# Performance work log

Measured on AMD Instinct MI355X. Metric: run time of the kernel, lower is better.

## Reference

```python
import jax, jax.numpy as jnp
import numpy as np
import math

D_MODEL = 256
SIGMA = 1.0


def _sinusoidal_pe(L, d_model, dtype=jnp.float32):
    # pe[l, 2i] = sin(l * w_i), pe[l, 2i+1] = cos(l * w_i)
    position = jnp.arange(L, dtype=dtype)[:, None]                       # [L,1]
    div_term = jnp.exp(jnp.arange(0, d_model, 2, dtype=dtype) * (-math.log(10000.0) / d_model))
    pe = jnp.zeros((L, d_model), dtype=dtype)
    pe = pe.at[:, 0::2].set(jnp.sin(position * div_term))
    pe = pe.at[:, 1::2].set(jnp.cos(position * div_term))
    return pe  # [L, d_model]


def setup_inputs() -> dict:
    key = jax.random.key(0)
    # scale 0.05 keeps pairwise sq-distances O(1) so S = exp(-d/2) is non-degenerate
    x = jax.random.normal(key, (4, 4096, 256), dtype=jnp.float32) * 0.05
    return {"x": x}


def reference(x):
    B, L, D = x.shape
    pe = _sinusoidal_pe(L, D_MODEL, dtype=x.dtype)[None]                 # [1,L,D]
    # pairwise squared distances via the expansion ||a||^2+||b||^2-2ab (avoids [B,L,L,D])
    sq = jnp.sum(x * x, axis=-1)                                         # [B,L]
    gram = jnp.einsum('bld,bmd->blm', x, x)                              # [B,L,L]
    dist_sq = jnp.maximum(sq[:, :, None] + sq[:, None, :] - 2.0 * gram, 0.0)
    S = jnp.exp(-dist_sq / (2.0 * SIGMA ** 2))                           # [B,L,L]
    sem = jnp.einsum('blm,bmd->bld', S, x) / jnp.sum(S, axis=-1, keepdims=True)
    return x + pe + sem
```

## Files before the change

kernel.cpp:

```cpp
#include <hip/hip_runtime.h>

typedef unsigned char u8;
typedef float f32x4 __attribute__((ext_vector_type(4)));
typedef float f32x16 __attribute__((ext_vector_type(16)));

#define LL 4096
#define PSTR 136
#define SCALE 16.0f
#define GSCALE (1.0f/256.0f)
#define FREQC (-0.03597789207803197f)

__device__ __forceinline__ long LCAST(uint2 v) { return __builtin_bit_cast(long, v); }

typedef __attribute__((address_space(3))) u8 lds_u8;
typedef __attribute__((address_space(1))) u8 glb_u8;
__device__ __forceinline__ void dma16(const u8* g, u8* l) {
  __builtin_amdgcn_global_load_lds((const glb_u8*)g, (lds_u8*)l, 16, 0, 0);
}

__global__ __launch_bounds__(256) void prep1(const float* __restrict__ x, u8* __restrict__ xbf,
                                             u8* __restrict__ xT, float* __restrict__ sq) {
  __shared__ u8 T[16 * 264];
  const int blk = blockIdx.x;
  const int b = blk >> 8, r0 = (blk & 255) << 4;
  const int tid = threadIdx.x;
  const long rowbase = (long)(b << 12) + r0;
  const float4* x4 = (const float4*)x + rowbase * 64;
  unsigned* xb4 = (unsigned*)xbf + rowbase * 64;
  #pragma unroll
  for (int i = 0; i < 4; ++i) {
    int idx = i * 256 + tid;
    float4 v = x4[idx];
    float s = v.x * v.x + v.y * v.y + v.z * v.z + v.w * v.w;
    #pragma unroll
    for (int o = 32; o; o >>= 1) s += __shfl_xor(s, o);
    int row = idx >> 6, dw = idx & 63;
    if ((tid & 63) == 0) sq[rowbase + row] = s;
    int pk = __builtin_amdgcn_cvt_pk_fp8_f32(v.x * SCALE, v.y * SCALE, 0, false);
    pk = __builtin_amdgcn_cvt_pk_fp8_f32(v.z * SCALE, v.w * SCALE, pk, true);
    int sdw = (((dw >> 1) ^ ((r0 + row) & 31)) << 1) | (dw & 1);
    xb4[row * 64 + sdw] = (unsigned)pk;
    *(unsigned*)(T + row * 264 + dw * 4) = (unsigned)pk;
  }
  __syncthreads();
  unsigned ob[4];
  #pragma unroll
  for (int jj = 0; jj < 4; ++jj) {
    unsigned b0 = T[(4 * jj + 0) * 264 + tid];
    unsigned b1 = T[(4 * jj + 1) * 264 + tid];
    unsigned b2 = T[(4 * jj + 2) * 264 + tid];
    unsigned b3 = T[(4 * jj + 3) * 264 + tid];
    ob[jj] = b0 | (b1 << 8) | (b2 << 16) | (b3 << 24);
  }
  u8* drow = xT + ((((long)(b << 8) + tid) << 12)) + ((r0 >> 7) << 7);
  const int cb = (r0 & 127) >> 3, key = tid & 15;
  *(uint2*)(drow + ((cb ^ key) << 3)) = *(uint2*)(ob);
  *(uint2*)(drow + (((cb + 1) ^ key) << 3)) = *(uint2*)(ob + 2);
}

__global__ __launch_bounds__(512, 2) void tpe_main(
    const u8* __restrict__ xbf, const u8* __restrict__ xT,
    const float* __restrict__ sqv,
    const float* __restrict__ x, float* __restrict__ out) {
  __shared__ u8 Kt[2][32768];
  __shared__ u8 Vt[2][32768];
  __shared__ u8 Ps[64 * PSTR];
  __shared__ float lred[8][64];
  __shared__ float linv[64];

  const int tid = threadIdx.x;
  const int w = tid >> 6;
  const int lane = tid & 63;
  const int l15 = lane & 15, l31 = lane & 31;
  const int q4 = lane >> 4;
  const int q2 = lane >> 5;

  const int blk = blockIdx.x;
  const int b = (blk & 7) >> 1;
  const int qt = ((blk >> 3) << 1) | (blk & 1);
  const int q0 = qt << 6;
  const long bL = (long)b * LL;

  uint2 qf[4][8];
  #pragma unroll
  for (int t = 0; t < 4; ++t) {
    const int row = q0 + 16 * t + l15;
    const u8* qrow = xbf + ((bL + row) << 8);
    const int key = row & 31;
    #pragma unroll
    for (int s = 0; s < 8; ++s)
      qf[t][s] = *(const uint2*)(qrow + (((q4 + 4 * s) ^ key) << 3));
  }
  float qa[4];
  #pragma unroll
  for (int t = 0; t < 4; ++t) qa[t] = -0.5f * sqv[bL + q0 + 16 * t + l15];

  f32x16 oacc[2];
  #pragma unroll
  for (int rb = 0; rb < 2; ++rb)
    #pragma unroll
    for (int k = 0; k < 16; ++k) oacc[rb][k] = 0.f;
  float rsacc[4] = {0.f, 0.f, 0.f, 0.f};

  const u8* kbat = xbf + (bL << 8);
  const long vbat = ((long)(b << 8)) << 12;

  #pragma unroll
  for (int c = 0; c < 4; ++c) {
    int idx = c * 512 + tid;
    dma16(kbat + idx * 16, &Kt[0][idx * 16]);
  }
  #pragma unroll
  for (int c = 0; c < 4; ++c) {
    int idx = c * 512 + tid;
    int d = idx >> 3, part = idx & 7;
    dma16(xT + vbat + ((long)d << 12) + part * 16, &Vt[0][idx * 16]);
  }
  __syncthreads();

  for (int it = 0; it < 32; ++it) {
    const int cur = it & 1;
    const int j0 = it << 7;
    if (it < 31) {
      const int g = it + 1;
      #pragma unroll
      for (int c = 0; c < 4; ++c) {
        int idx = c * 512 + tid;
        dma16(kbat + ((long)g << 15) + idx * 16, &Kt[cur ^ 1][idx * 16]);
      }
      #pragma unroll
      for (int c = 0; c < 4; ++c) {
        int idx = c * 512 + tid;
        int d = idx >> 3, part = idx & 7;
        dma16(xT + vbat + ((long)d << 12) + g * 128 + part * 16, &Vt[cur ^ 1][idx * 16]);
      }
    }
    float4 skv4 = *(const float4*)(sqv + bL + j0 + 16 * w + 4 * q4);
    const u8* kt = Kt[cur];
    const int krow = 16 * w + l15;
    const int kkey = krow & 31;
    f32x4 sacc[4];
    #pragma unroll
    for (int t = 0; t < 4; ++t) {
      sacc[t][0] = 0.f; sacc[t][1] = 0.f; sacc[t][2] = 0.f; sacc[t][3] = 0.f;
    }
    #pragma unroll
    for (int s = 0; s < 8; ++s) {
      uint2 kf = *(const uint2*)(kt + krow * 256 + (((q4 + 4 * s) ^ kkey) << 3));
      long av = LCAST(kf);
      #pragma unroll
      for (int t = 0; t < 4; ++t)
        sacc[t] = __builtin_amdgcn_mfma_f32_16x16x32_fp8_fp8(av, LCAST(qf[t][s]), sacc[t], 0, 0, 0);
    }
    #pragma unroll
    for (int t = 0; t < 4; ++t) {
      float p0 = __expf(fminf(fmaf(sacc[t][0], GSCALE, qa[t] + skv4.x), 0.f));
      float p1 = __expf(fminf(fmaf(sacc[t][1], GSCALE, qa[t] + skv4.y), 0.f));
      float p2 = __expf(fminf(fmaf(sacc[t][2], GSCALE, qa[t] + skv4.z), 0.f));
      float p3 = __expf(fminf(fmaf(sacc[t][3], GSCALE, qa[t] + skv4.w), 0.f));
      rsacc[t] += (p0 + p1) + (p2 + p3);
      int pk = __builtin_amdgcn_cvt_pk_fp8_f32(p0, p1, 0, false);
      pk = __builtin_amdgcn_cvt_pk_fp8_f32(p2, p3, pk, true);
      *(int*)(Ps + (16 * t + l15) * PSTR + 16 * w + 4 * q4) = pk;
    }
    __syncthreads();
    const u8* vt = Vt[cur];
    const int vkey = l31 & 15;
    const u8* vrow = vt + (32 * w + l31) * 128;
    #pragma unroll
    for (int s = 0; s < 8; ++s) {
      uint2 bv = *(const uint2*)(vrow + (((2 * s + q2) ^ vkey) << 3));
      long bvl = LCAST(bv);
      #pragma unroll
      for (int rb = 0; rb < 2; ++rb) {
        long a = *(const long*)(Ps + (32 * rb + l31) * PSTR + 16 * s + 8 * q2);
        oacc[rb] = __builtin_amdgcn_mfma_f32_32x32x16_fp8_fp8(a, bvl, oacc[rb], 0, 0, 0);
      }
    }
    __syncthreads();
  }

  #pragma unroll
  for (int t = 0; t < 4; ++t) {
    float r = rsacc[t];
    r += __shfl_xor(r, 16);
    r += __shfl_xor(r, 32);
    if (lane < 16) lred[w][16 * t + lane] = r;
  }
  __syncthreads();
  if (tid < 64) {
    float s = 0.f;
    #pragma unroll
    for (int ww = 0; ww < 8; ++ww) s += lred[ww][tid];
    linv[tid] = 0.0625f / s;
  }
  __syncthreads();
  const int col = 32 * w + l31;
  const float freq = __expf((float)(col & ~1) * FREQC);
  #pragma unroll
  for (int rb = 0; rb < 2; ++rb) {
    #pragma unroll
    for (int reg = 0; reg < 16; ++reg) {
      int row = 32 * rb + 4 * q2 + (reg & 3) + 8 * (reg >> 2);
      int l = q0 + row;
      float ang = (float)l * freq;
      float pv = (col & 1) ? __cosf(ang) : __sinf(ang);
      long off = ((bL + l) << 8) + col;
      out[off] = oacc[rb][reg] * linv[row] + x[off] + pv;
    }
  }
}

extern "C" void kernel_launch(void* const* d_in, const int* in_sizes, int n_in,
                              void* d_out, int out_size, void* d_ws, size_t ws_size,
                              hipStream_t stream) {
  const float* x = (const float*)d_in[0];
  float* out = (float*)d_out;
  char* ws = (char*)d_ws;
  u8* xbf = (u8*)ws;
  u8* xT = (u8*)(ws + 4194304);
  float* sq = (float*)(ws + 8388608);
  prep1<<<1024, 256, 0, stream>>>(x, xbf, xT, sq);
  tpe_main<<<256, 512, 0, stream>>>(xbf, xT, sq, x, out);
}
```

Before: 149.5 us.

## Halve query and key tile sizes to double grid and raise occupancy

Reduces each block to 32 query rows and 64-key K/V tiles, shrinking LDS so up to four blocks fit per CU, and launches twice as many blocks. Warps are re-split into 2 row groups by 4 key groups for the S tile, and the V tile swizzle and addressing are reworked for 64-byte rows. This aims to fill more CUs and hide latency. In exchange, each K/V tile is reused by fewer query rows, so global and L2 traffic roughly doubles and there are more barriers per key.

After: 161.7 us. +8.2%, slower.

```diff
diff --git a/kernel.cpp b/kernel.cpp
--- a/kernel.cpp
+++ b/kernel.cpp
@@ -5,7 +5,7 @@
 typedef float f32x16 __attribute__((ext_vector_type(16)));
 
 #define LL 4096
-#define PSTR 136
+#define PSTR 72
 #define SCALE 16.0f
 #define GSCALE (1.0f/256.0f)
 #define FREQC (-0.03597789207803197f)
@@ -58,15 +58,15 @@
   *(uint2*)(drow + (((cb + 1) ^ key) << 3)) = *(uint2*)(ob + 2);
 }
 
-__global__ __launch_bounds__(512, 2) void tpe_main(
+__global__ __launch_bounds__(512, 4) void tpe_main(
     const u8* __restrict__ xbf, const u8* __restrict__ xT,
     const float* __restrict__ sqv,
     const float* __restrict__ x, float* __restrict__ out) {
-  __shared__ u8 Kt[2][32768];
-  __shared__ u8 Vt[2][32768];
-  __shared__ u8 Ps[64 * PSTR];
-  __shared__ float lred[8][64];
-  __shared__ float linv[64];
+  __shared__ u8 Kt[2][16384];
+  __shared__ u8 Vt[2][16384];
+  __shared__ u8 Ps[32 * PSTR];
+  __shared__ float lred[8][32];
+  __shared__ float linv[32];
 
   const int tid = threadIdx.x;
   const int w = tid >> 6;
@@ -74,140 +74,125 @@
   const int l15 = lane & 15, l31 = lane & 31;
   const int q4 = lane >> 4;
   const int q2 = lane >> 5;
+  const int wj = w & 3;
+  const int wi = w >> 2;
 
   const int blk = blockIdx.x;
   const int b = (blk & 7) >> 1;
   const int qt = ((blk >> 3) << 1) | (blk & 1);
-  const int q0 = qt << 6;
+  const int q0 = qt << 5;
   const long bL = (long)b * LL;
 
-  uint2 qf[4][8];
-  #pragma unroll
-  for (int t = 0; t < 4; ++t) {
-    const int row = q0 + 16 * t + l15;
+  uint2 qf[8];
+  {
+    const int row = q0 + 16 * wi + l15;
     const u8* qrow = xbf + ((bL + row) << 8);
     const int key = row & 31;
     #pragma unroll
     for (int s = 0; s < 8; ++s)
-      qf[t][s] = *(const uint2*)(qrow + (((q4 + 4 * s) ^ key) << 3));
-  }
-  float qa[4];
-  #pragma unroll
-  for (int t = 0; t < 4; ++t) qa[t] = -0.5f * sqv[bL + q0 + 16 * t + l15];
-
-  f32x16 oacc[2];
-  #pragma unroll
-  for (int rb = 0; rb < 2; ++rb)
-    #pragma unroll
-    for (int k = 0; k < 16; ++k) oacc[rb][k] = 0.f;
-  float rsacc[4] = {0.f, 0.f, 0.f, 0.f};
+      qf[s] = *(const uint2*)(qrow + (((q4 + 4 * s) ^ key) << 3));
+  }
+  const float qa = -0.5f * sqv[bL + q0 + 16 * wi + l15];
+
+  f32x16 oacc;
+  #pragma unroll
+  for (int k = 0; k < 16; ++k) oacc[k] = 0.f;
+  float rsacc = 0.f;
 
   const u8* kbat = xbf + (bL << 8);
   const long vbat = ((long)(b << 8)) << 12;
 
   #pragma unroll
-  for (int c = 0; c < 4; ++c) {
+  for (int c = 0; c < 2; ++c) {
     int idx = c * 512 + tid;
     dma16(kbat + idx * 16, &Kt[0][idx * 16]);
   }
   #pragma unroll
-  for (int c = 0; c < 4; ++c) {
+  for (int c = 0; c < 2; ++c) {
     int idx = c * 512 + tid;
-    int d = idx >> 3, part = idx & 7;
-    dma16(xT + vbat + ((long)d << 12) + part * 16, &Vt[0][idx * 16]);
-  }
-  __syncthreads();
-
-  for (int it = 0; it < 32; ++it) {
+    int d = idx >> 2, c16 = idx & 3;
+    dma16(xT + vbat + ((long)d << 12) + (((d >> 3) & 1) << 6) + c16 * 16, &Vt[0][idx * 16]);
+  }
+  __syncthreads();
+
+  for (int it = 0; it < 64; ++it) {
     const int cur = it & 1;
-    const int j0 = it << 7;
-    if (it < 31) {
+    const int j0 = it << 6;
+    if (it < 63) {
       const int g = it + 1;
+      const int jn = g << 6;
       #pragma unroll
-      for (int c = 0; c < 4; ++c) {
+      for (int c = 0; c < 2; ++c) {
         int idx = c * 512 + tid;
-        dma16(kbat + ((long)g << 15) + idx * 16, &Kt[cur ^ 1][idx * 16]);
+        dma16(kbat + ((long)g << 14) + idx * 16, &Kt[cur ^ 1][idx * 16]);
       }
+      const int sg = jn >> 7, h = (jn >> 6) & 1;
       #pragma unroll
-      for (int c = 0; c < 4; ++c) {
+      for (int c = 0; c < 2; ++c) {
         int idx = c * 512 + tid;
-        int d = idx >> 3, part = idx & 7;
-        dma16(xT + vbat + ((long)d << 12) + g * 128 + part * 16, &Vt[cur ^ 1][idx * 16]);
+        int d = idx >> 2, c16 = idx & 3;
+        dma16(xT + vbat + ((long)d << 12) + sg * 128 + (((h ^ (d >> 3)) & 1) << 6) + c16 * 16,
+              &Vt[cur ^ 1][idx * 16]);
       }
     }
-    float4 skv4 = *(const float4*)(sqv + bL + j0 + 16 * w + 4 * q4);
+    float4 skv4 = *(const float4*)(sqv + bL + j0 + 16 * wj + 4 * q4);
     const u8* kt = Kt[cur];
-    const int krow = 16 * w + l15;
+    const int krow = 16 * wj + l15;
     const int kkey = krow & 31;
-    f32x4 sacc[4];
-    #pragma unroll
-    for (int t = 0; t < 4; ++t) {
-      sacc[t][0] = 0.f; sacc[t][1] = 0.f; sacc[t][2] = 0.f; sacc[t][3] = 0.f;
-    }
+    f32x4 sacc;
+    sacc[0] = 0.f; sacc[1] = 0.f; sacc[2] = 0.f; sacc[3] = 0.f;
     #pragma unroll
     for (int s = 0; s < 8; ++s) {
       uint2 kf = *(const uint2*)(kt + krow * 256 + (((q4 + 4 * s) ^ kkey) << 3));
-      long av = LCAST(kf);
-      #pragma unroll
-      for (int t = 0; t < 4; ++t)
-        sacc[t] = __builtin_amdgcn_mfma_f32_16x16x32_fp8_fp8(av, LCAST(qf[t][s]), sacc[t], 0, 0, 0);
-    }
-    #pragma unroll
-    for (int t = 0; t < 4; ++t) {
-      float p0 = __expf(fminf(fmaf(sacc[t][0], GSCALE, qa[t] + skv4.x), 0.f));
-      float p1 = __expf(fminf(fmaf(sacc[t][1], GSCALE, qa[t] + skv4.y), 0.f));
-      float p2 = __expf(fminf(fmaf(sacc[t][2], GSCALE, qa[t] + skv4.z), 0.f));
-      float p3 = __expf(fminf(fmaf(sacc[t][3], GSCALE, qa[t] + skv4.w), 0.f));
-      rsacc[t] += (p0 + p1) + (p2 + p3);
+      sacc = __builtin_amdgcn_mfma_f32_16x16x32_fp8_fp8(LCAST(kf), LCAST(qf[s]), sacc, 0, 0, 0);
+    }
+    {
+      float p0 = __expf(fminf(fmaf(sacc[0], GSCALE, qa + skv4.x), 0.f));
+      float p1 = __expf(fminf(fmaf(sacc[1], GSCALE, qa + skv4.y), 0.f));
+      float p2 = __expf(fminf(fmaf(sacc[2], GSCALE, qa + skv4.z), 0.f));
+      float p3 = __expf(fminf(fmaf(sacc[3], GSCALE, qa + skv4.w), 0.f));
+      rsacc += (p0 + p1) + (p2 + p3);
       int pk = __builtin_amdgcn_cvt_pk_fp8_f32(p0, p1, 0, false);
       pk = __builtin_amdgcn_cvt_pk_fp8_f32(p2, p3, pk, true);
-      *(int*)(Ps + (16 * t + l15) * PSTR + 16 * w + 4 * q4) = pk;
+      *(int*)(Ps + (16 * wi + l15) * PSTR + 16 * wj + 4 * q4) = pk;
     }
     __syncthreads();
     const u8* vt = Vt[cur];
-    const int vkey = l31 & 15;
-    const u8* vrow = vt + (32 * w + l31) * 128;
-    #pragma unroll
-    for (int s = 0; s < 8; ++s) {
+    const int d = 32 * w + l31;
+    const u8* vrow = vt + ((32 * w + l31) << 6);
+    const int vkey = l31 & 7;
+    #pragma unroll
+    for (int s = 0; s < 4; ++s) {
       uint2 bv = *(const uint2*)(vrow + (((2 * s + q2) ^ vkey) << 3));
-      long bvl = LCAST(bv);
-      #pragma unroll
-      for (int rb = 0; rb < 2; ++rb) {
-        long a = *(const long*)(Ps + (32 * rb + l31) * PSTR + 16 * s + 8 * q2);
-        oacc[rb] = __builtin_amdgcn_mfma_f32_32x32x16_fp8_fp8(a, bvl, oacc[rb], 0, 0, 0);
-      }
+      long a = *(const long*)(Ps + l31 * PSTR + 16 * s + 8 * q2);
+      oacc = __builtin_amdgcn_mfma_f32_32x32x16_fp8_fp8(a, LCAST(bv), oacc, 0, 0, 0);
     }
     __syncthreads();
   }
 
-  #pragma unroll
-  for (int t = 0; t < 4; ++t) {
-    float r = rsacc[t];
+  {
+    float r = rsacc;
     r += __shfl_xor(r, 16);
     r += __shfl_xor(r, 32);
-    if (lane < 16) lred[w][16 * t + lane] = r;
-  }
-  __syncthreads();
-  if (tid < 64) {
-    float s = 0.f;
-    #pragma unroll
-    for (int ww = 0; ww < 8; ++ww) s += lred[ww][tid];
+    if (lane < 16) lred[w][16 * wi + l15] = r;
+  }
+  __syncthreads();
+  if (tid < 32) {
+    const int wb = (tid >> 4) << 2;
+    float s = lred[wb][tid] + lred[wb + 1][tid] + lred[wb + 2][tid] + lred[wb + 3][tid];
     linv[tid] = 0.0625f / s;
   }
   __syncthreads();
   const int col = 32 * w + l31;
   const float freq = __expf((float)(col & ~1) * FREQC);
   #pragma unroll
-  for (int rb = 0; rb < 2; ++rb) {
-    #pragma unroll
-    for (int reg = 0; reg < 16; ++reg) {
-      int row = 32 * rb + 4 * q2 + (reg & 3) + 8 * (reg >> 2);
-      int l = q0 + row;
-      float ang = (float)l * freq;
-      float pv = (col & 1) ? __cosf(ang) : __sinf(ang);
-      long off = ((bL + l) << 8) + col;
-      out[off] = oacc[rb][reg] * linv[row] + x[off] + pv;
-    }
+  for (int reg = 0; reg < 16; ++reg) {
+    int row = 4 * q2 + (reg & 3) + 8 * (reg >> 2);
+    int l = q0 + row;
+    float ang = (float)l * freq;
+    float pv = (col & 1) ? __cosf(ang) : __sinf(ang);
+    long off = ((bL + l) << 8) + col;
+    out[off] = oacc[reg] * linv[row] + x[off] + pv;
   }
 }
 
@@ -221,5 +206,5 @@
   u8* xT = (u8*)(ws + 4194304);
   float* sq = (float*)(ws + 8388608);
   prep1<<<1024, 256, 0, stream>>>(x, xbf, xT, sq);
-  tpe_main<<<256, 512, 0, stream>>>(xbf, xT, sq, x, out);
-}
+  tpe_main<<<512, 512, 0, stream>>>(xbf, xT, sq, x, out);
+}
```

## Software-pipeline PV matmul one step behind QK and load V straight into registers

Applied to the files above, without the earlier changes.

Removes the shared-memory V tile. Each wave now loads its own V fragments directly from global memory into registers, double-buffered across iterations. The P tile is double-buffered, so the PV MFMAs for the previous block run in the same phase as the QK MFMAs for the current block, which drops one __syncthreads per iteration. The loop is manually unrolled by two to alternate buffers, with a drain step at the end. This trades LDS traffic and a barrier for more VGPR pressure and uncoalesced 8-byte global loads of V.

Result: faster. 139.7 us (-6.5%).

```diff
diff --git a/kernel.cpp b/kernel.cpp
--- a/kernel.cpp
+++ b/kernel.cpp
@@ -63,8 +63,7 @@
     const float* __restrict__ sqv,
     const float* __restrict__ x, float* __restrict__ out) {
   __shared__ u8 Kt[2][32768];
-  __shared__ u8 Vt[2][32768];
-  __shared__ u8 Ps[64 * PSTR];
+  __shared__ u8 Ps[2][64 * PSTR];
   __shared__ float lred[8][64];
   __shared__ float linv[64];
 
@@ -82,6 +81,7 @@
   const long bL = (long)b * LL;
 
   uint2 qf[4][8];
+  float qa[4];
   #pragma unroll
   for (int t = 0; t < 4; ++t) {
     const int row = q0 + 16 * t + l15;
@@ -90,10 +90,8 @@
     #pragma unroll
     for (int s = 0; s < 8; ++s)
       qf[t][s] = *(const uint2*)(qrow + (((q4 + 4 * s) ^ key) << 3));
-  }
-  float qa[4];
-  #pragma unroll
-  for (int t = 0; t < 4; ++t) qa[t] = -0.5f * sqv[bL + q0 + 16 * t + l15];
+    qa[t] = -0.5f * sqv[bL + row];
+  }
 
   f32x16 oacc[2];
   #pragma unroll
@@ -103,81 +101,88 @@
   float rsacc[4] = {0.f, 0.f, 0.f, 0.f};
 
   const u8* kbat = xbf + (bL << 8);
-  const long vbat = ((long)(b << 8)) << 12;
+  const u8* vseg = xT + (((long)(b << 8) + 32 * w + l31) << 12);
+  const int vkey = l31 & 15;
+
+  uint2 vfA[8], vfB[8];
 
   #pragma unroll
   for (int c = 0; c < 4; ++c) {
-    int idx = c * 512 + tid;
-    dma16(kbat + idx * 16, &Kt[0][idx * 16]);
-  }
-  #pragma unroll
-  for (int c = 0; c < 4; ++c) {
-    int idx = c * 512 + tid;
-    int d = idx >> 3, part = idx & 7;
-    dma16(xT + vbat + ((long)d << 12) + part * 16, &Vt[0][idx * 16]);
-  }
-  __syncthreads();
-
-  for (int it = 0; it < 32; ++it) {
-    const int cur = it & 1;
-    const int j0 = it << 7;
-    if (it < 31) {
-      const int g = it + 1;
-      #pragma unroll
-      for (int c = 0; c < 4; ++c) {
-        int idx = c * 512 + tid;
-        dma16(kbat + ((long)g << 15) + idx * 16, &Kt[cur ^ 1][idx * 16]);
-      }
-      #pragma unroll
-      for (int c = 0; c < 4; ++c) {
-        int idx = c * 512 + tid;
-        int d = idx >> 3, part = idx & 7;
-        dma16(xT + vbat + ((long)d << 12) + g * 128 + part * 16, &Vt[cur ^ 1][idx * 16]);
-      }
-    }
-    float4 skv4 = *(const float4*)(sqv + bL + j0 + 16 * w + 4 * q4);
-    const u8* kt = Kt[cur];
-    const int krow = 16 * w + l15;
-    const int kkey = krow & 31;
-    f32x4 sacc[4];
-    #pragma unroll
-    for (int t = 0; t < 4; ++t) {
-      sacc[t][0] = 0.f; sacc[t][1] = 0.f; sacc[t][2] = 0.f; sacc[t][3] = 0.f;
-    }
-    #pragma unroll
-    for (int s = 0; s < 8; ++s) {
-      uint2 kf = *(const uint2*)(kt + krow * 256 + (((q4 + 4 * s) ^ kkey) << 3));
-      long av = LCAST(kf);
-      #pragma unroll
-      for (int t = 0; t < 4; ++t)
-        sacc[t] = __builtin_amdgcn_mfma_f32_16x16x32_fp8_fp8(av, LCAST(qf[t][s]), sacc[t], 0, 0, 0);
-    }
-    #pragma unroll
-    for (int t = 0; t < 4; ++t) {
-      float p0 = __expf(fminf(fmaf(sacc[t][0], GSCALE, qa[t] + skv4.x), 0.f));
-      float p1 = __expf(fminf(fmaf(sacc[t][1], GSCALE, qa[t] + skv4.y), 0.f));
-      float p2 = __expf(fminf(fmaf(sacc[t][2], GSCALE, qa[t] + skv4.z), 0.f));
-      float p3 = __expf(fminf(fmaf(sacc[t][3], GSCALE, qa[t] + skv4.w), 0.f));
-      rsacc[t] += (p0 + p1) + (p2 + p3);
-      int pk = __builtin_amdgcn_cvt_pk_fp8_f32(p0, p1, 0, false);
-      pk = __builtin_amdgcn_cvt_pk_fp8_f32(p2, p3, pk, true);
-      *(int*)(Ps + (16 * t + l15) * PSTR + 16 * w + 4 * q4) = pk;
-    }
-    __syncthreads();
-    const u8* vt = Vt[cur];
-    const int vkey = l31 & 15;
-    const u8* vrow = vt + (32 * w + l31) * 128;
-    #pragma unroll
-    for (int s = 0; s < 8; ++s) {
-      uint2 bv = *(const uint2*)(vrow + (((2 * s + q2) ^ vkey) << 3));
-      long bvl = LCAST(bv);
-      #pragma unroll
-      for (int rb = 0; rb < 2; ++rb) {
-        long a = *(const long*)(Ps + (32 * rb + l31) * PSTR + 16 * s + 8 * q2);
-        oacc[rb] = __builtin_amdgcn_mfma_f32_32x32x16_fp8_fp8(a, bvl, oacc[rb], 0, 0, 0);
-      }
-    }
-    __syncthreads();
+    int off = c * 8192 + tid * 16;
+    dma16(kbat + off, Kt[0] + off);
+  }
+  __syncthreads();
+
+#define TPE_ITER(IT, KCUR, KNXT, PPREV, PCUR, VFC, VFN)                                     \
+  {                                                                                         \
+    const int j0 = (IT) << 7;                                                               \
+    if ((IT) < 31) {    \
+      const u8* ks = kbat + ((long)((IT) + 1) << 15);                                       \
+      _Pragma("unroll")                                                                     \
+      for (int c = 0; c < 4; ++c) {                                                         \
+        int off = c * 8192 + tid * 16;                                                      \
+        dma16(ks + off, (KNXT) + off);                                                      \
+      }                                                                                     \
+    }                                                                                       \
+    float4 skv4 = *(const float4*)(sqv + bL + j0 + 16 * w + 4 * q4);                        \
+    if ((IT) != 0) {           \
+      _Pragma("unroll")                                                                     \
+      for (int s = 0; s < 8; ++s) {                                                         \
+        long a0 = *(const long*)((PPREV) + l31 * PSTR + 16 * s + 8 * q2);                   \
+        long a1 = *(const long*)((PPREV) + (32 + l31) * PSTR + 16 * s + 8 * q2);            \
+        long bv = LCAST(VFC[s]);                                                            \
+        oacc[0] = __builtin_amdgcn_mfma_f32_32x32x16_fp8_fp8(a0, bv, oacc[0], 0, 0, 0);     \
+        oacc[1] = __builtin_amdgcn_mfma_f32_32x32x16_fp8_fp8(a1, bv, oacc[1], 0, 0, 0);     \
+      }                                                                                     \
+    }                                                                                       \
+    _Pragma("unroll")              \
+    for (int s = 0; s < 8; ++s)                                                             \
+      VFN[s] = *(const uint2*)(vseg + j0 + (((2 * s + q2) ^ vkey) << 3));                   \
+    {                        \
+      const int krow = 16 * w + l15;                                                        \
+      const int kkey = krow & 31;                                                           \
+      const u8* kb2 = (KCUR) + krow * 256;                                                  \
+      f32x4 sacc[4];                                                                        \
+      _Pragma("unroll")                                                                     \
+      for (int t = 0; t < 4; ++t) {                                                         \
+        sacc[t][0] = 0.f; sacc[t][1] = 0.f; sacc[t][2] = 0.f; sacc[t][3] = 0.f;             \
+      }                                                                                     \
+      _Pragma("unroll")                                                                     \
+      for (int s = 0; s < 8; ++s) {                                                         \
+        uint2 kf = *(const uint2*)(kb2 + (((q4 + 4 * s) ^ kkey) << 3));                     \
+        long av = LCAST(kf);                                                                \
+        _Pragma("unroll")                                                                   \
+        for (int t = 0; t < 4; ++t)                                                         \
+          sacc[t] = __builtin_amdgcn_mfma_f32_16x16x32_fp8_fp8(av, LCAST(qf[t][s]), sacc[t], 0, 0, 0); \
+      }                                                                                     \
+      _Pragma("unroll")        \
+      for (int t = 0; t < 4; ++t) {                 \
+        float p0 = __expf(fminf(fmaf(sacc[t][0], GSCALE, qa[t] + skv4.x), 0.f));            \
+        float p1 = __expf(fminf(fmaf(sacc[t][1], GSCALE, qa[t] + skv4.y), 0.f));            \
+        float p2 = __expf(fminf(fmaf(sacc[t][2], GSCALE, qa[t] + skv4.z), 0.f));            \
+        float p3 = __expf(fminf(fmaf(sacc[t][3], GSCALE, qa[t] + skv4.w), 0.f));            \
+        rsacc[t] += (p0 + p1) + (p2 + p3);                                                  \
+        int pk = __builtin_amdgcn_cvt_pk_fp8_f32(p0, p1, 0, false);                         \
+        pk = __builtin_amdgcn_cvt_pk_fp8_f32(p2, p3, pk, true);                             \
+        *(int*)((PCUR) + (16 * t + l15) * PSTR + 16 * w + 4 * q4) = pk;                     \
+      }                                                                                     \
+    }                                                                                       \
+    __syncthreads();         \
+  }
+
+  for (int it2 = 0; it2 < 16; ++it2) {
+    TPE_ITER(2 * it2,     Kt[0], Kt[1], Ps[1], Ps[0], vfA, vfB)
+    TPE_ITER(2 * it2 + 1, Kt[1], Kt[0], Ps[0], Ps[1], vfB, vfA)
+  }
+#undef TPE_ITER
+
+  #pragma unroll
+  for (int s = 0; s < 8; ++s) {
+    long a0 = *(const long*)(Ps[1] + l31 * PSTR + 16 * s + 8 * q2);
+    long a1 = *(const long*)(Ps[1] + (32 + l31) * PSTR + 16 * s + 8 * q2);
+    long bv = LCAST(vfA[s]);
+    oacc[0] = __builtin_amdgcn_mfma_f32_32x32x16_fp8_fp8(a0, bv, oacc[0], 0, 0, 0);
+    oacc[1] = __builtin_amdgcn_mfma_f32_32x32x16_fp8_fp8(a1, bv, oacc[1], 0, 0, 0);
   }
 
   #pragma unroll
@@ -185,7 +190,7 @@
     float r = rsacc[t];
     r += __shfl_xor(r, 16);
     r += __shfl_xor(r, 32);
-    if (lane < 16) lred[w][16 * t + lane] = r;
+    if (lane < 16) lred[w][16 * t + l15] = r;
   }
   __syncthreads();
   if (tid < 64) {
```
